# Kernel tuning notes

Hardware: AMD Instinct MI355X
Metric: run time of the kernel (lower is better)

## Reference

```python
import jax, jax.numpy as jnp
import numpy as np

B, V, E = 32, 2048, 12288
IMG_F = 512
GCN_DIMS = [(3 + IMG_F, 512), (512, 512), (512, 512), (512, 512), (512, 64), (64, 3)]
FC_DIMS = [(V * 3, 1024), (1024, 1024), (1024, V * 3)]


def setup_inputs() -> dict:
    key = jax.random.key(0)
    ks = jax.random.split(key, 3 + len(GCN_DIMS) + len(FC_DIMS))
    inp = {}
    inp["vertices"] = jax.random.normal(ks[0], (B, V, 3), dtype=jnp.float32)
    inp["img_features"] = jax.random.normal(ks[1], (B, IMG_F), dtype=jnp.float32)
    inp["edge_index"] = jax.random.randint(ks[2], (2, E), 0, V, dtype=jnp.int32)
    for i, (fi, fo) in enumerate(GCN_DIMS):
        inp[f"W{i+1}"] = (jax.random.normal(ks[3 + i], (fi, fo), dtype=jnp.float32) / np.sqrt(fi)).astype(jnp.float32)
        inp[f"b{i+1}"] = jnp.zeros((fo,), dtype=jnp.float32)
    for i, (fi, fo) in enumerate(FC_DIMS):
        inp[f"fcW{i+1}"] = (jax.random.normal(ks[3 + len(GCN_DIMS) + i], (fi, fo), dtype=jnp.float32) / np.sqrt(fi)).astype(jnp.float32)
        inp[f"fcb{i+1}"] = jnp.zeros((fo,), dtype=jnp.float32)
    return inp


def _gcn_norm(edge_index):
    # PyG GCNConv: add self-loops, symmetric normalization 1/sqrt(d_i d_j).
    loop = jnp.arange(V, dtype=edge_index.dtype)
    src = jnp.concatenate([edge_index[0], loop])
    dst = jnp.concatenate([edge_index[1], loop])
    deg = jax.ops.segment_sum(jnp.ones_like(dst, dtype=jnp.float32), dst, num_segments=V)
    dinv = jax.lax.rsqrt(deg)  # deg >= 1 due to self-loops
    norm = dinv[src] * dinv[dst]  # [E+V]
    return src, dst, norm


def _gcn_layer(x, W, b, src, dst, norm):
    # x: [B, V, Fin] -> [B, V, Fout]; transform then gather/scatter aggregate.
    h = jnp.einsum("bvi,io->bvo", x, W)
    msg = h[:, src, :] * norm[None, :, None]          # gather over edges
    agg = jax.vmap(lambda m: jax.ops.segment_sum(m, dst, num_segments=V))(msg)
    return agg + b


def reference(vertices, img_features, edge_index,
              W1, b1, W2, b2, W3, b3, W4, b4, W5, b5, W6, b6,
              fcW1, fcb1, fcW2, fcb2, fcW3, fcb3):
    src, dst, norm = _gcn_norm(edge_index)
    # concat vertex coords with broadcast image feature: [B, V, 3+512]
    x = jnp.concatenate([vertices, jnp.broadcast_to(img_features[:, None, :], (B, V, IMG_F))], axis=2)
    x = _gcn_layer(x, W1, b1, src, dst, norm)
    x = _gcn_layer(x, W2, b2, src, dst, norm)
    x = jax.nn.relu(x)
    x = _gcn_layer(x, W3, b3, src, dst, norm)
    x = _gcn_layer(x, W4, b4, src, dst, norm)
    x = jax.nn.relu(x)
    x = _gcn_layer(x, W5, b5, src, dst, norm)
    x = _gcn_layer(x, W6, b6, src, dst, norm)
    x = jax.nn.relu(x)
    x = x.reshape(B, V * 3)
    h = x @ fcW1 + fcb1
    h = h @ fcW2 + fcb2
    h = jnp.tanh(h @ fcW3 + fcb3)
    deformations = h.reshape(B, V, 3) * 0.1
    return vertices + deformations
```

## Files before the change

### kernel.cpp

```cpp
#include <hip/hip_runtime.h>
#include <stdint.h>
#include <math.h>

#define B_ 32
#define V_ 2048
#define E_ 12288
#define M_ (B_*V_)

typedef __bf16 bf16x8 __attribute__((ext_vector_type(8)));
typedef float f32x4 __attribute__((ext_vector_type(4)));

__device__ __forceinline__ float bf2f(unsigned short u){
  union { unsigned int i; float f; } v; v.i = ((unsigned int)u) << 16; return v.f;
}
__device__ __forceinline__ unsigned short f2bf(float f){
  union { float f; unsigned int i; } v; v.f = f;
  unsigned int r = (v.i + 0x7fffu + ((v.i >> 16) & 1u)) >> 16;
  return (unsigned short)r;
}
__device__ __forceinline__ void gload16(const unsigned short* g, unsigned short* l){
  __builtin_amdgcn_global_load_lds(
      (const __attribute__((address_space(1))) void*)g,
      (__attribute__((address_space(3))) void*)l, 16, 0, 0);
}

__global__ __launch_bounds__(1024) void k_pre0(
    const int* __restrict__ ei, int* __restrict__ rowptr_g, int* __restrict__ cols_g,
    float* __restrict__ vals_g, float* __restrict__ selfw_g,
    float* __restrict__ wsum_g, float* __restrict__ w2_g,
    const float* __restrict__ W3, const float* __restrict__ W4,
    const float* __restrict__ img, const float* __restrict__ W1,
    unsigned short* __restrict__ W3B, unsigned short* __restrict__ W4T,
    float* __restrict__ partB){
  __shared__ int   sdeg[V_];
  __shared__ int   srp[V_ + 1];
  __shared__ int   sfill[V_];
  __shared__ float sdinv[V_];
  __shared__ float swsum[V_];
  __shared__ float sw2[V_];
  __shared__ int   swt[16];
  __shared__ __align__(16) float tile[4][32][33];
  if (blockIdx.x == 0){
    const int t = threadIdx.x;
    sdeg[2*t] = 0; sdeg[2*t+1] = 0; sfill[2*t] = 0; sfill[2*t+1] = 0;
    __syncthreads();
    #pragma unroll
    for (int e = t; e < E_; e += 1024) atomicAdd(&sdeg[ei[E_ + e]], 1);
    __syncthreads();
    int c0 = sdeg[2*t], c1 = sdeg[2*t+1];
    int s2 = c0 + c1;
    int lane = t & 63, wid = t >> 6;
    int pre = s2;
    #pragma unroll
    for (int off = 1; off < 64; off <<= 1){
      int u = __shfl_up(pre, off);
      if (lane >= off) pre += u;
    }
    if (lane == 63) swt[wid] = pre;
    __syncthreads();
    if (t == 0){
      int run = 0;
      #pragma unroll
      for (int i = 0; i < 16; i++){ int x = swt[i]; swt[i] = run; run += x; }
      srp[V_] = run;
    }
    __syncthreads();
    int base = swt[wid] + (pre - s2);
    srp[2*t] = base; srp[2*t+1] = base + c0;
    #pragma unroll
    for (int v = t; v < V_; v += 1024){
      float d = (float)(sdeg[v] + 1);
      float di = rsqrtf(d);
      sdinv[v] = di;
      swsum[v] = di * di;
    }
    __syncthreads();
    #pragma unroll
    for (int e = t; e < E_; e += 1024){
      int s = ei[e], d = ei[E_ + e];
      int pos = srp[d] + atomicAdd(&sfill[d], 1);
      float val = sdinv[s] * sdinv[d];
      cols_g[pos] = s;
      vals_g[pos] = val;
      atomicAdd(&swsum[d], val);
    }
    __syncthreads();
    #pragma unroll
    for (int v = t; v < V_; v += 1024)
      sw2[v] = (sdinv[v] * sdinv[v]) * swsum[v];
    __syncthreads();
    #pragma unroll
    for (int e = t; e < E_; e += 1024){
      int s = ei[e], d = ei[E_ + e];
      atomicAdd(&sw2[d], sdinv[s] * sdinv[d] * swsum[s]);
    }
    __syncthreads();
    #pragma unroll
    for (int v = t; v < V_; v += 1024){
      rowptr_g[v] = srp[v];
      selfw_g[v]  = sdinv[v] * sdinv[v];
      wsum_g[v]   = swsum[v];
      w2_g[v]     = sw2[v];
    }
    if (t == 0) rowptr_g[V_] = srp[V_];
  } else {
    int u = blockIdx.x - 1;
    int t10 = threadIdx.x;
    int sub = (u << 2) + (t10 >> 8);
    int t = t10 & 255;
    int ti = t10 >> 8;
    if (sub < 256){
      int tr0 = (sub >> 4) << 5, tc0 = (sub & 15) << 5;
      int r = t >> 5, c = t & 31;
      #pragma unroll
      for (int i = 0; i < 4; i++)
        tile[ti][r + 8*i][c] = W4[(size_t)(tr0 + r + 8*i) * 512 + tc0 + c];
      __syncthreads();
      #pragma unroll
      for (int i = 0; i < 4; i++)
        W4T[(size_t)(tc0 + r + 8*i) * 512 + tr0 + c] = f2bf(tile[ti][c][r + 8*i]);
    } else if (sub < 256 + 1024){
      int id = (sub - 256) * 256 + t;
      W3B[id] = f2bf(W3[id]);
    } else {
      int g = sub - 1280;
      int kc = g >> 1, nh = g & 1;
      int k0 = kc * 16;
      float* xs = &tile[ti][0][0];
      for (int i = t; i < 512; i += 256)
        xs[i] = img[(size_t)(i >> 4) * 512 + k0 + (i & 15)];
      __syncthreads();
      const float* W = W1 + 3 * 512;
      int n = (nh << 8) + t;
      float acc[32] = {};
      #pragma unroll
      for (int kg = 0; kg < 4; kg++){
        const float* wp = W + (size_t)(k0 + kg * 4) * 512 + n;
        float w0 = wp[0], w1 = wp[512], w2 = wp[1024], w3 = wp[1536];
        #pragma unroll
        for (int r = 0; r < 32; r++){
          f32x4 xv = *(const f32x4*)&xs[r * 16 + kg * 4];
          acc[r] += xv[0]*w0 + xv[1]*w1 + xv[2]*w2 + xv[3]*w3;
        }
      }
      float* p = partB + (size_t)kc * 16384 + n;
      #pragma unroll
      for (int r = 0; r < 32; r++) p[(size_t)r * 512] = acc[r];
    }
  }
}

__global__ __launch_bounds__(256) void k_preB(
    const float* __restrict__ partB, float* __restrict__ I1,
    const float* __restrict__ b3, const float* __restrict__ W4,
    const float* __restrict__ W5, const float* __restrict__ W6,
    const float* __restrict__ b5,
    float* __restrict__ C34, float* __restrict__ W56, float* __restrict__ C56){
  int blk = blockIdx.x, t = threadIdx.x;
  if (blk < 64){
    int id = blk * 256 + t;
    float a = 0.f;
    #pragma unroll
    for (int s = 0; s < 32; s++) a += partB[(size_t)s * 16384 + id];
    I1[id] = a;
  } else {
    int id = (blk - 64) * 256 + t;
    if (id < 512){
      float a0=0,a1=0,a2=0,a3=0;
      for (int k = 0; k < 512; k += 4){
        a0 += b3[k]   * W4[(size_t)k * 512 + id];
        a1 += b3[k+1] * W4[(size_t)(k+1) * 512 + id];
        a2 += b3[k+2] * W4[(size_t)(k+2) * 512 + id];
        a3 += b3[k+3] * W4[(size_t)(k+3) * 512 + id];
      }
      C34[id] = a0+a1+a2+a3;
    } else if (id < 512 + 1536){
      int i = id - 512; int k5 = i / 3, j = i % 3;
      float a = 0.f;
      #pragma unroll 4
      for (int u = 0; u < 64; u++) a += W5[k5 * 64 + u] * W6[u * 3 + j];
      W56[i] = a;
    } else if (id < 512 + 1536 + 3){
      int j = id - (512 + 1536);
      float a = 0.f;
      #pragma unroll 4
      for (int u = 0; u < 64; u++) a += b5[u] * W6[u * 3 + j];
      C56[j] = a;
    }
  }
}

__global__ __launch_bounds__(256) void k_preC(
    const float* __restrict__ b1, const float* __restrict__ W1,
    const float* __restrict__ I1, const float* __restrict__ W2,
    float* __restrict__ partB){
  __shared__ __align__(16) float xs[36 * 16];
  int g = blockIdx.x;
  int kc = g >> 1, k0 = kc * 16;
  int t = threadIdx.x;
  int n = ((g & 1) << 8) + t;
  for (int i = t; i < 576; i += 256){
    int r = i >> 4, kk = i & 15;
    const float* q;
    if (r == 0)      q = b1;
    else if (r < 4)  q = W1 + (size_t)(r - 1) * 512;
    else             q = I1 + (size_t)(r - 4) * 512;
    xs[i] = q[k0 + kk];
  }
  __syncthreads();
  float acc[36] = {};
  #pragma unroll
  for (int kg = 0; kg < 4; kg++){
    const float* wp = W2 + (size_t)(k0 + kg * 4) * 512 + n;
    float w0 = wp[0], w1 = wp[512], w2 = wp[1024], w3 = wp[1536];
    #pragma unroll
    for (int r = 0; r < 36; r++){
      f32x4 xv = *(const f32x4*)&xs[r * 16 + kg * 4];
      acc[r] += xv[0]*w0 + xv[1]*w1 + xv[2]*w2 + xv[3]*w3;
    }
  }
  float* p = partB + (size_t)kc * 18432 + n;
  #pragma unroll
  for (int r = 0; r < 36; r++) p[(size_t)r * 512] = acc[r];
}

__global__ __launch_bounds__(256) void k_preD(
    const float* __restrict__ partB, float* __restrict__ P){
  int id = blockIdx.x * 256 + threadIdx.x;
  float a = 0.f;
  #pragma unroll
  for (int s = 0; s < 32; s++) a += partB[(size_t)s * 18432 + id];
  P[id] = a;
}

__global__ __launch_bounds__(1024) void k_va2(
    const float* __restrict__ in, const int* __restrict__ rowptr,
    const int* __restrict__ cols, const float* __restrict__ vals,
    const float* __restrict__ selfw, float* __restrict__ outv){
  __shared__ float xs[V_ * 3];
  __shared__ float ys[V_ * 3];
  int b = blockIdx.x, t = threadIdx.x;
  const float* ib = in + (size_t)b * V_ * 3;
  for (int i = t; i < V_ * 3; i += 1024) xs[i] = ib[i];
  __syncthreads();
  for (int v = t; v < V_; v += 1024){
    float sw = selfw[v];
    float a0 = sw * xs[v*3], a1 = sw * xs[v*3+1], a2 = sw * xs[v*3+2];
    int re = rowptr[v + 1];
    for (int e = rowptr[v]; e < re; e++){
      int s = cols[e]; float vv = vals[e];
      a0 += vv * xs[s*3]; a1 += vv * xs[s*3+1]; a2 += vv * xs[s*3+2];
    }
    ys[v*3] = a0; ys[v*3+1] = a1; ys[v*3+2] = a2;
  }
  __syncthreads();
  for (int v = t; v < V_; v += 1024){
    float sw = selfw[v];
    float a0 = sw * ys[v*3], a1 = sw * ys[v*3+1], a2 = sw * ys[v*3+2];
    int re = rowptr[v + 1];
    for (int e = rowptr[v]; e < re; e++){
      int s = cols[e]; float vv = vals[e];
      a0 += vv * ys[s*3]; a1 += vv * ys[s*3+1]; a2 += vv * ys[s*3+2];
    }
    float* o = outv + ((size_t)v * 32 + b) * 3;
    o[0] = a0; o[1] = a1; o[2] = a2;
  }
}

__global__ __launch_bounds__(1024) void k_x2(
    const float* __restrict__ va2v, const float* __restrict__ P,
    const float* __restrict__ wsum, const float* __restrict__ w2s,
    const float* __restrict__ b2,
    unsigned short* __restrict__ Y){
  int v = (blockIdx.x << 2) + (threadIdx.x >> 8);
  int batch = (blockIdx.y << 2) + ((threadIdx.x >> 6) & 3);
  int f8 = (threadIdx.x & 63) * 8;
  const float* va = va2v + ((size_t)v * 32 + batch) * 3;
  float x0 = va[0], x1 = va[1], x2 = va[2];
  float w2v = w2s[v], wsv = wsum[v];
  float tt[8];
  #pragma unroll
  for (int h = 0; h < 2; h++){
    f32x4 wv0 = *(const f32x4*)&P[512  + f8 + 4*h];
    f32x4 wv1 = *(const f32x4*)&P[1024 + f8 + 4*h];
    f32x4 wv2 = *(const f32x4*)&P[1536 + f8 + 4*h];
    f32x4 ccv = *(const f32x4*)&P[f8 + 4*h];
    f32x4 bbv = *(const f32x4*)&b2[f8 + 4*h];
    f32x4 iiv = *(const f32x4*)&P[2048 + (size_t)batch * 512 + f8 + 4*h];
    #pragma unroll
    for (int j = 0; j < 4; j++){
      float tv = x0*wv0[j] + x1*wv1[j] + x2*wv2[j] + w2v*iiv[j] + wsv*ccv[j] + bbv[j];
      tt[4*h + j] = fmaxf(tv, 0.f);
    }
  }
  unsigned int o[4];
  #pragma unroll
  for (int i = 0; i < 4; i++)
    o[i] = (unsigned int)f2bf(tt[2*i]) | ((unsigned int)f2bf(tt[2*i+1]) << 16);
  *(uint4*)&Y[((size_t)v * 32 + batch) * 512 + f8] = *(uint4*)o;
}

__global__ __launch_bounds__(256) void k_aggb(
    const unsigned short* __restrict__ Hg, const int* __restrict__ rowptr,
    const int* __restrict__ cols, const float* __restrict__ vals,
    const float* __restrict__ selfw, unsigned short* __restrict__ Xo){
  int dst = blockIdx.x;
  int batch = (blockIdx.y << 2) + (threadIdx.x >> 6);
  int f8 = (threadIdx.x & 63) * 8;
  int rs = rowptr[dst], re = rowptr[dst + 1];
  float sw = selfw[dst];
  float a[8];
  {
    uint4 q = *(const uint4*)&Hg[((size_t)dst * 32 + batch) * 512 + f8];
    const unsigned int* w = (const unsigned int*)&q;
    #pragma unroll
    for (int i = 0; i < 4; i++){
      a[2*i]   = sw * bf2f(w[i] & 0xffff);
      a[2*i+1] = sw * bf2f(w[i] >> 16);
    }
  }
  int e = rs;
  for (; e + 1 < re; e += 2){
    int s0 = cols[e], s1 = cols[e+1];
    float v0 = vals[e], v1 = vals[e+1];
    uint4 q0 = *(const uint4*)&Hg[((size_t)s0 * 32 + batch) * 512 + f8];
    uint4 q1 = *(const uint4*)&Hg[((size_t)s1 * 32 + batch) * 512 + f8];
    const unsigned int* w0 = (const unsigned int*)&q0;
    const unsigned int* w1 = (const unsigned int*)&q1;
    #pragma unroll
    for (int i = 0; i < 4; i++){
      a[2*i]   += v0 * bf2f(w0[i] & 0xffff) + v1 * bf2f(w1[i] & 0xffff);
      a[2*i+1] += v0 * bf2f(w0[i] >> 16)    + v1 * bf2f(w1[i] >> 16);
    }
  }
  if (e < re){
    int s = cols[e]; float v = vals[e];
    uint4 q = *(const uint4*)&Hg[((size_t)s * 32 + batch) * 512 + f8];
    const unsigned int* w = (const unsigned int*)&q;
    #pragma unroll
    for (int i = 0; i < 4; i++){
      a[2*i]   += v * bf2f(w[i] & 0xffff);
      a[2*i+1] += v * bf2f(w[i] >> 16);
    }
  }
  unsigned int o[4];
  #pragma unroll
  for (int i = 0; i < 4; i++)
    o[i] = (unsigned int)f2bf(a[2*i]) | ((unsigned int)f2bf(a[2*i+1]) << 16);
  *(uint4*)&Xo[((size_t)dst * 32 + batch) * 512 + f8] = *(uint4*)o;
}

template<int BM, int BN, int WM, int WN, int TM, int TN>
__global__ __launch_bounds__(WM*WN*64) void k_gemm(
    const unsigned short* __restrict__ Xg, const unsigned short* __restrict__ Wt,
    unsigned short* __restrict__ Hg, int K, int N,
    const float* __restrict__ wsumv, const float* __restrict__ cvec,
    const float* __restrict__ bias, int relu,
    const float* __restrict__ W56g, float* __restrict__ h5p){
  constexpr int BK = 32;
  constexpr int NW = WM * WN;
  constexpr int NT = NW * 64;
  constexpr int RA = BM / NW;
  constexpr int RB = BN / NW;
  __shared__ __align__(16) unsigned short As[2][BM * BK];
  __shared__ __align__(16) unsigned short Bs[2][BN * BK];
  __shared__ float h5s[BM * 3];
  const int tid = threadIdx.x;
  const int row0 = blockIdx.x * BM, col0 = blockIdx.y * BN;
  const int wave = tid >> 6, lane = tid & 63;
  const int wr = wave / WN, wc = wave % WN;
  const int lrow = lane & 15, lq = lane >> 4;
  const int lrw = lane >> 2, lcol = (lane & 3) * 8;
  const int arow = wave * RA, brow = wave * RB;
  if (h5p){
    for (int i = tid; i < BM * 3; i += NT) h5s[i] = 0.f;
  }
  f32x4 acc[TM][TN] = {};
  #pragma unroll
  for (int t = 0; t < RA / 16; t++)
    gload16(&Xg[(size_t)(row0 + arow + t * 16 + lrw) * K + lcol],
            &As[0][(arow + t * 16) * BK]);
  #pragma unroll
  for (int t = 0; t < RB / 16; t++)
    gload16(&Wt[(size_t)(col0 + brow + t * 16 + lrw) * K + lcol],
            &Bs[0][(brow + t * 16) * BK]);
  int cur = 0;
  for (int k0 = 0; k0 < K; k0 += BK){
    __syncthreads();
    if (k0 + BK < K){
      #pragma unroll
      for (int t = 0; t < RA / 16; t++)
        gload16(&Xg[(size_t)(row0 + arow + t * 16 + lrw) * K + k0 + BK + lcol],
                &As[cur ^ 1][(arow + t * 16) * BK]);
      #pragma unroll
      for (int t = 0; t < RB / 16; t++)
        gload16(&Wt[(size_t)(col0 + brow + t * 16 + lrw) * K + k0 + BK + lcol],
                &Bs[cur ^ 1][(brow + t * 16) * BK]);
    }
    bf16x8 af[TM], bfr[TN];
    #pragma unroll
    for (int tm = 0; tm < TM; tm++)
      af[tm] = *(const bf16x8*)&As[cur][(wr * TM * 16 + tm * 16 + lrow) * BK + lq * 8];
    #pragma unroll
    for (int tn = 0; tn < TN; tn++)
      bfr[tn] = *(const bf16x8*)&Bs[cur][(wc * TN * 16 + tn * 16 + lrow) * BK + lq * 8];
    #pragma unroll
    for (int tm = 0; tm < TM; tm++)
      #pragma unroll
      for (int tn = 0; tn < TN; tn++)
        acc[tm][tn] = __builtin_amdgcn_mfma_f32_16x16x32_bf16(af[tm], bfr[tn], acc[tm][tn], 0, 0, 0);
    cur ^= 1;
  }
  if (h5p){
    float w56l[TN][3], cvl[TN], bvl[TN];
    #pragma unroll
    for (int tn = 0; tn < TN; tn++){
      int col = col0 + wc * TN * 16 + tn * 16 + lrow;
      cvl[tn] = cvec[col]; bvl[tn] = bias[col];
      w56l[tn][0] = W56g[col * 3];
      w56l[tn][1] = W56g[col * 3 + 1];
      w56l[tn][2] = W56g[col * 3 + 2];
    }
    #pragma unroll
    for (int tm = 0; tm < TM; tm++){
      #pragma unroll
      for (int r = 0; r < 4; r++){
        int lr = wr * TM * 16 + tm * 16 + lq * 4 + r;
        float ws = wsumv[(row0 + lr) >> 5];
        float p0 = 0.f, p1 = 0.f, p2 = 0.f;
        #pragma unroll
        for (int tn = 0; tn < TN; tn++){
          float x = fmaxf(acc[tm][tn][r] + ws * cvl[tn] + bvl[tn], 0.f);
          p0 += x * w56l[tn][0]; p1 += x * w56l[tn][1]; p2 += x * w56l[tn][2];
        }
        #pragma unroll
        for (int off = 8; off; off >>= 1){
          p0 += __shfl_down(p0, off);
          p1 += __shfl_down(p1, off);
          p2 += __shfl_down(p2, off);
        }
        if (lrow == 0){
          atomicAdd(&h5s[lr * 3 + 0], p0);
          atomicAdd(&h5s[lr * 3 + 1], p1);
          atomicAdd(&h5s[lr * 3 + 2], p2);
        }
      }
    }
    __syncthreads();
    float* dst = h5p + (size_t)blockIdx.y * ((size_t)M_ * 3) + (size_t)row0 * 3;
    for (int i = tid; i < BM * 3; i += NT) dst[i] = h5s[i];
  } else {
    #pragma unroll
    for (int tm = 0; tm < TM; tm++){
      #pragma unroll
      for (int tn = 0; tn < TN; tn++){
        int col = col0 + wc * TN * 16 + tn * 16 + lrow;
        float cv = 0.f, bv = 0.f;
        if (cvec){ cv = cvec[col]; bv = bias[col]; }
        #pragma unroll
        for (int r = 0; r < 4; r++){
          int row = row0 + wr * TM * 16 + tm * 16 + lq * 4 + r;
          float x = acc[tm][tn][r];
          if (cvec) x += wsumv[row >> 5] * cv + bv;
          if (relu) x = fmaxf(x, 0.f);
          Hg[(size_t)row * N + col] = f2bf(x);
        }
      }
    }
  }
}

__global__ __launch_bounds__(1024) void k_xa2(
    const float* __restrict__ h5p, const int* __restrict__ rowptr,
    const int* __restrict__ cols, const float* __restrict__ vals,
    const float* __restrict__ selfw, const float* __restrict__ wsum,
    const float* __restrict__ C56, const float* __restrict__ b6,
    float* __restrict__ XF){
  __shared__ float xs[V_ * 3];
  __shared__ float ys[V_ * 3];
  int b = blockIdx.x, t = threadIdx.x;
  const size_t M3 = (size_t)M_ * 3;
  for (int i = t; i < V_ * 3; i += 1024){
    int v = i / 3, j = i - v * 3;
    size_t g = ((size_t)v * 32 + b) * 3 + j;
    xs[i] = h5p[g] + h5p[M3 + g] + h5p[2 * M3 + g] + h5p[3 * M3 + g];
  }
  __syncthreads();
  for (int v = t; v < V_; v += 1024){
    float sw = selfw[v];
    float a0 = sw * xs[v*3], a1 = sw * xs[v*3+1], a2 = sw * xs[v*3+2];
    int re = rowptr[v + 1];
    for (int e = rowptr[v]; e < re; e++){
      int s = cols[e]; float vv = vals[e];
      a0 += vv * xs[s*3]; a1 += vv * xs[s*3+1]; a2 += vv * xs[s*3+2];
    }
    ys[v*3] = a0; ys[v*3+1] = a1; ys[v*3+2] = a2;
  }
  __syncthreads();
  float* ob = XF + (size_t)b * V_ * 3;
  for (int v = t; v < V_; v += 1024){
    float sw = selfw[v];
    float a0 = sw * ys[v*3], a1 = sw * ys[v*3+1], a2 = sw * ys[v*3+2];
    int re = rowptr[v + 1];
    for (int e = rowptr[v]; e < re; e++){
      int s = cols[e]; float vv = vals[e];
      a0 += vv * ys[s*3]; a1 += vv * ys[s*3+1]; a2 += vv * ys[s*3+2];
    }
    float w = wsum[v];
    a0 = fmaxf(a0 + w * C56[0] + b6[0], 0.f);
    a1 = fmaxf(a1 + w * C56[1] + b6[1], 0.f);
    a2 = fmaxf(a2 + w * C56[2] + b6[2], 0.f);
    ob[v*3] = a0; ob[v*3+1] = a1; ob[v*3+2] = a2;
  }
}

template<int R, int KC>
__global__ __launch_bounds__(256) void k_fcp(
    const float* __restrict__ in, const float* __restrict__ W,
    float* __restrict__ partial, int K, int N){
  const int n = blockIdx.x * 256 + threadIdx.x;
  const int k0 = blockIdx.y * KC;
  float acc[R] = {};
  for (int kk = 0; kk < KC; kk += 4){
    const float* wp = W + (size_t)(k0 + kk) * N + n;
    float w0 = wp[0];
    float w1 = wp[(size_t)N];
    float w2 = wp[(size_t)2 * N];
    float w3 = wp[(size_t)3 * N];
    #pragma unroll
    for (int r = 0; r < R; r++){
      const float* xp = in + (size_t)r * K + k0 + kk;
      acc[r] += xp[0]*w0 + xp[1]*w1 + xp[2]*w2 + xp[3]*w3;
    }
  }
  float* p = partial + (size_t)blockIdx.y * R * N + n;
  #pragma unroll
  for (int r = 0; r < R; r++) p[(size_t)r * N] = acc[r];
}

__global__ __launch_bounds__(256) void k_fcr(
    const float* __restrict__ partial, const float* __restrict__ bias,
    float* __restrict__ out, int total, int N, int KS, int mode,
    const float* __restrict__ vert){
  int id = blockIdx.x * 256 + threadIdx.x;
  if (id >= total) return;
  int n = id % N;
  float a0 = 0.f, a1 = 0.f, a2 = 0.f, a3 = 0.f;
  int s = 0;
  for (; s + 4 <= KS; s += 4){
    a0 += partial[(size_t)s * total + id];
    a1 += partial[(size_t)(s + 1) * total + id];
    a2 += partial[(size_t)(s + 2) * total + id];
    a3 += partial[(size_t)(s + 3) * total + id];
  }
  for (; s < KS; s++) a0 += partial[(size_t)s * total + id];
  float acc = a0 + a1 + a2 + a3;
  if (bias) acc += bias[n];
  if (mode) acc = vert[id] + 0.1f * tanhf(acc);
  out[id] = acc;
}

static constexpr size_t AL(size_t x){ return (x + 255) & ~(size_t)255; }
static constexpr size_t S512 = (size_t)M_ * 512 * 2;
static constexpr size_t S3   = (size_t)M_ * 3 * 4;
static constexpr size_t OXA  = 0;
static constexpr size_t OXB  = OXA  + AL(S512);
static constexpr size_t OVA2 = OXB  + AL(S512);
static constexpr size_t OH5P = OVA2 + AL(S3);
static constexpr size_t OXF  = OH5P + AL(4 * S3);
static constexpr size_t OFC1 = OXF  + AL(S3);
static constexpr size_t OFC2 = OFC1 + AL((size_t)B_ * 1024 * 4);
static constexpr size_t OI1  = OFC2 + AL((size_t)B_ * 1024 * 4);
static constexpr size_t OP   = OI1  + AL((size_t)32 * 512 * 4);
static constexpr size_t OC34 = OP   + AL((size_t)36 * 512 * 4);
static constexpr size_t OW56 = OC34 + AL((size_t)512 * 4);
static constexpr size_t OC56 = OW56 + AL((size_t)512 * 3 * 4);
static constexpr size_t OW3B = OC56 + AL((size_t)3 * 4);
static constexpr size_t OW4T = OW3B + AL((size_t)512 * 512 * 2);
static constexpr size_t OW34 = OW4T + AL((size_t)512 * 512 * 2);
static constexpr size_t OROW = OW34 + AL((size_t)512 * 512 * 2);
static constexpr size_t OCOL = OROW + AL((size_t)(V_ + 1) * 4);
static constexpr size_t OVAL = OCOL + AL((size_t)E_ * 4);
static constexpr size_t OSELF= OVAL + AL((size_t)E_ * 4);
static constexpr size_t OWS  = OSELF+ AL((size_t)V_ * 4);
static constexpr size_t OW2S = OWS  + AL((size_t)V_ * 4);

extern "C" void kernel_launch(void* const* d_in, const int* in_sizes, int n_in,
                              void* d_out, int out_size, void* d_ws, size_t ws_size,
                              hipStream_t stream){
  const float* vert  = (const float*)d_in[0];
  const float* img   = (const float*)d_in[1];
  const int*   ei    = (const int*)  d_in[2];
  const float* W1 = (const float*)d_in[3],  *b1 = (const float*)d_in[4];
  const float* W2 = (const float*)d_in[5],  *b2 = (const float*)d_in[6];
  const float* W3 = (const float*)d_in[7],  *b3 = (const float*)d_in[8];
  const float* W4 = (const float*)d_in[9],  *b4 = (const float*)d_in[10];
  const float* W5 = (const float*)d_in[11], *b5 = (const float*)d_in[12];
  const float* W6 = (const float*)d_in[13], *b6 = (const float*)d_in[14];
  const float* fcW1 = (const float*)d_in[15], *fcb1 = (const float*)d_in[16];
  const float* fcW2 = (const float*)d_in[17], *fcb2 = (const float*)d_in[18];
  const float* fcW3 = (const float*)d_in[19], *fcb3 = (const float*)d_in[20];
  float* out = (float*)d_out;

  char* ws = (char*)d_ws;
  unsigned short* XA  = (unsigned short*)(ws + OXA);
  unsigned short* XB  = (unsigned short*)(ws + OXB);
  float* VA2v = (float*)(ws + OVA2);
  float* H5P  = (float*)(ws + OH5P);
  float* XF   = (float*)(ws + OXF);
  float* FC1o = (float*)(ws + OFC1);
  float* FC2o = (float*)(ws + OFC2);
  float* I1   = (float*)(ws + OI1);
  float* P    = (float*)(ws + OP);
  float* C34  = (float*)(ws + OC34);
  float* W56  = (float*)(ws + OW56);
  float* C56  = (float*)(ws + OC56);
  unsigned short* W3B = (unsigned short*)(ws + OW3B);
  unsigned short* W4T = (unsigned short*)(ws + OW4T);
  unsigned short* W34 = (unsigned short*)(ws + OW34);
  float* PARTA = (float*)(ws + OXA);
  float* PARTB = (float*)(ws + OXB);
  int*   ROW  = (int*)(ws + OROW);
  int*   COL  = (int*)(ws + OCOL);
  float* VAL  = (float*)(ws + OVAL);
  float* SELF = (float*)(ws + OSELF);
  float* WSUM = (float*)(ws + OWS);
  float* W2S  = (float*)(ws + OW2S);

  k_pre0<<<337, 1024, 0, stream>>>(ei, ROW, COL, VAL, SELF, WSUM, W2S,
                                   W3, W4, img, W1, W3B, W4T, PARTB);
  k_preB<<<64 + 9, 256, 0, stream>>>(PARTB, I1, b3, W4, W5, W6, b5, C34, W56, C56);
  k_preC<<<64, 256, 0, stream>>>(b1, W1, I1, W2, PARTB);
  k_preD<<<72, 256, 0, stream>>>(PARTB, P);
  k_gemm<64,64,2,2,2,2><<<dim3(8, 8), 256, 0, stream>>>(W4T, W3B, W34, 512, 512,
                                                        nullptr, nullptr, nullptr, 0,
                                                        nullptr, nullptr);

  k_va2<<<B_, 1024, 0, stream>>>(vert, ROW, COL, VAL, SELF, VA2v);
  k_x2<<<dim3(V_ / 4, 8), 1024, 0, stream>>>(VA2v, P, WSUM, W2S, b2, XA);
  k_aggb<<<dim3(V_, 8), 256, 0, stream>>>(XA, ROW, COL, VAL, SELF, XB);
  k_aggb<<<dim3(V_, 8), 256, 0, stream>>>(XB, ROW, COL, VAL, SELF, XA);

  k_gemm<128,128,2,2,4,4><<<dim3(M_ / 128, 4), 256, 0, stream>>>(XA, W34, XB, 512, 512,
                                                                 WSUM, C34, b4, 1,
                                                                 W56, H5P);

  k_xa2<<<B_, 1024, 0, stream>>>(H5P, ROW, COL, VAL, SELF, WSUM, C56, b6, XF);

  k_fcp<32,64><<<dim3(4, 96), 256, 0, stream>>>(XF, fcW1, PARTA, 6144, 1024);
  k_fcr<<<(B_ * 1024 + 255) / 256, 256, 0, stream>>>(PARTA, fcb1, FC1o, 32 * 1024, 1024, 96, 0, nullptr);
  k_fcp<32,64><<<dim3(4, 16), 256, 0, stream>>>(FC1o, fcW2, PARTA, 1024, 1024);
  k_fcr<<<(B_ * 1024 + 255) / 256, 256, 0, stream>>>(PARTA, fcb2, FC2o, 32 * 1024, 1024, 16, 0, nullptr);
  k_fcp<32,64><<<dim3(24, 16), 256, 0, stream>>>(FC2o, fcW3, PARTA, 1024, 6144);
  k_fcr<<<(B_ * 6144 + 255) / 256, 256, 0, stream>>>(PARTA, fcb3, out, 32 * 6144, 6144, 16, 1, vert);
}
```

Baseline: 582.7 us.

## Fuse two sparse aggregation passes into one LDS-resident kernel per feature chunk

Replaces the two back-to-back global-memory gather/scatter aggregation launches with a single kernel. Each block loads a 16-feature slice for one batch across all vertices into LDS, runs both aggregation hops out of shared memory, and writes only the final result. This removes the intermediate global round trip and the random global gathers. In exchange it uses 128KB of LDS per 1024-thread block, which limits occupancy, and each block walks the full CSR once per hop.

```diff
diff --git a/kernel.cpp b/kernel.cpp
--- a/kernel.cpp
+++ b/kernel.cpp
@@ -300,54 +300,110 @@
   *(uint4*)&Y[((size_t)v * 32 + batch) * 512 + f8] = *(uint4*)o;
 }
 
-__global__ __launch_bounds__(256) void k_aggb(
+__global__ __launch_bounds__(1024) void k_agg2(
     const unsigned short* __restrict__ Hg, const int* __restrict__ rowptr,
     const int* __restrict__ cols, const float* __restrict__ vals,
     const float* __restrict__ selfw, unsigned short* __restrict__ Xo){
-  int dst = blockIdx.x;
-  int batch = (blockIdx.y << 2) + (threadIdx.x >> 6);
-  int f8 = (threadIdx.x & 63) * 8;
-  int rs = rowptr[dst], re = rowptr[dst + 1];
-  float sw = selfw[dst];
-  float a[8];
-  {
-    uint4 q = *(const uint4*)&Hg[((size_t)dst * 32 + batch) * 512 + f8];
-    const unsigned int* w = (const unsigned int*)&q;
-    #pragma unroll
-    for (int i = 0; i < 4; i++){
-      a[2*i]   = sw * bf2f(w[i] & 0xffff);
-      a[2*i+1] = sw * bf2f(w[i] >> 16);
-    }
-  }
-  int e = rs;
-  for (; e + 1 < re; e += 2){
-    int s0 = cols[e], s1 = cols[e+1];
-    float v0 = vals[e], v1 = vals[e+1];
-    uint4 q0 = *(const uint4*)&Hg[((size_t)s0 * 32 + batch) * 512 + f8];
-    uint4 q1 = *(const uint4*)&Hg[((size_t)s1 * 32 + batch) * 512 + f8];
-    const unsigned int* w0 = (const unsigned int*)&q0;
-    const unsigned int* w1 = (const unsigned int*)&q1;
-    #pragma unroll
-    for (int i = 0; i < 4; i++){
-      a[2*i]   += v0 * bf2f(w0[i] & 0xffff) + v1 * bf2f(w1[i] & 0xffff);
-      a[2*i+1] += v0 * bf2f(w0[i] >> 16)    + v1 * bf2f(w1[i] >> 16);
-    }
-  }
-  if (e < re){
-    int s = cols[e]; float v = vals[e];
-    uint4 q = *(const uint4*)&Hg[((size_t)s * 32 + batch) * 512 + f8];
-    const unsigned int* w = (const unsigned int*)&q;
-    #pragma unroll
-    for (int i = 0; i < 4; i++){
-      a[2*i]   += v * bf2f(w[i] & 0xffff);
-      a[2*i+1] += v * bf2f(w[i] >> 16);
-    }
-  }
-  unsigned int o[4];
-  #pragma unroll
-  for (int i = 0; i < 4; i++)
-    o[i] = (unsigned int)f2bf(a[2*i]) | ((unsigned int)f2bf(a[2*i+1]) << 16);
-  *(uint4*)&Xo[((size_t)dst * 32 + batch) * 512 + f8] = *(uint4*)o;
+  __shared__ __align__(16) unsigned short xs[V_ * 16];
+  __shared__ __align__(16) unsigned short ys[V_ * 16];
+  const int fc = blockIdx.x;
+  const int b  = blockIdx.y;
+  const int t = threadIdx.x;
+  for (int i = t; i < V_ * 2; i += 1024){
+    int v = i >> 1, h = (i & 1) << 3;
+    *(uint4*)&xs[v * 16 + h] =
+        *(const uint4*)&Hg[((size_t)v * 32 + b) * 512 + fc * 16 + h];
+  }
+  __syncthreads();
+  for (int i = t; i < V_ * 2; i += 1024){
+    int dst = i >> 1, h = (i & 1) << 3;
+    float sw = selfw[dst];
+    float a[8];
+    {
+      uint4 q = *(const uint4*)&xs[dst * 16 + h];
+      const unsigned int* w = (const unsigned int*)&q;
+      #pragma unroll
+      for (int k = 0; k < 4; k++){
+        a[2*k]   = sw * bf2f(w[k] & 0xffff);
+        a[2*k+1] = sw * bf2f(w[k] >> 16);
+      }
+    }
+    int rs = rowptr[dst], re = rowptr[dst + 1];
+    int e = rs;
+    for (; e + 1 < re; e += 2){
+      int s0 = cols[e], s1 = cols[e+1];
+      float v0 = vals[e], v1 = vals[e+1];
+      uint4 q0 = *(const uint4*)&xs[s0 * 16 + h];
+      uint4 q1 = *(const uint4*)&xs[s1 * 16 + h];
+      const unsigned int* w0 = (const unsigned int*)&q0;
+      const unsigned int* w1 = (const unsigned int*)&q1;
+      #pragma unroll
+      for (int k = 0; k < 4; k++){
+        a[2*k]   += v0 * bf2f(w0[k] & 0xffff) + v1 * bf2f(w1[k] & 0xffff);
+        a[2*k+1] += v0 * bf2f(w0[k] >> 16)    + v1 * bf2f(w1[k] >> 16);
+      }
+    }
+    if (e < re){
+      int s = cols[e]; float v = vals[e];
+      uint4 q = *(const uint4*)&xs[s * 16 + h];
+      const unsigned int* w = (const unsigned int*)&q;
+      #pragma unroll
+      for (int k = 0; k < 4; k++){
+        a[2*k]   += v * bf2f(w[k] & 0xffff);
+        a[2*k+1] += v * bf2f(w[k] >> 16);
+      }
+    }
+    unsigned int o[4];
+    #pragma unroll
+    for (int k = 0; k < 4; k++)
+      o[k] = (unsigned int)f2bf(a[2*k]) | ((unsigned int)f2bf(a[2*k+1]) << 16);
+    *(uint4*)&ys[dst * 16 + h] = *(uint4*)o;
+  }
+  __syncthreads();
+  for (int i = t; i < V_ * 2; i += 1024){
+    int dst = i >> 1, h = (i & 1) << 3;
+    float sw = selfw[dst];
+    float a[8];
+    {
+      uint4 q = *(const uint4*)&ys[dst * 16 + h];
+      const unsigned int* w = (const unsigned int*)&q;
+      #pragma unroll
+      for (int k = 0; k < 4; k++){
+        a[2*k]   = sw * bf2f(w[k] & 0xffff);
+        a[2*k+1] = sw * bf2f(w[k] >> 16);
+      }
+    }
+    int rs = rowptr[dst], re = rowptr[dst + 1];
+    int e = rs;
+    for (; e + 1 < re; e += 2){
+      int s0 = cols[e], s1 = cols[e+1];
+      float v0 = vals[e], v1 = vals[e+1];
+      uint4 q0 = *(const uint4*)&ys[s0 * 16 + h];
+      uint4 q1 = *(const uint4*)&ys[s1 * 16 + h];
+      const unsigned int* w0 = (const unsigned int*)&q0;
+      const unsigned int* w1 = (const unsigned int*)&q1;
+      #pragma unroll
+      for (int k = 0; k < 4; k++){
+        a[2*k]   += v0 * bf2f(w0[k] & 0xffff) + v1 * bf2f(w1[k] & 0xffff);
+        a[2*k+1] += v0 * bf2f(w0[k] >> 16)    + v1 * bf2f(w1[k] >> 16);
+      }
+    }
+    if (e < re){
+      int s = cols[e]; float v = vals[e];
+      uint4 q = *(const uint4*)&ys[s * 16 + h];
+      const unsigned int* w = (const unsigned int*)&q;
+      #pragma unroll
+      for (int k = 0; k < 4; k++){
+        a[2*k]   += v * bf2f(w[k] & 0xffff);
+        a[2*k+1] += v * bf2f(w[k] >> 16);
+      }
+    }
+    unsigned int o[4];
+    #pragma unroll
+    for (int k = 0; k < 4; k++)
+      o[k] = (unsigned int)f2bf(a[2*k]) | ((unsigned int)f2bf(a[2*k+1]) << 16);
+    *(uint4*)&Xo[((size_t)dst * 32 + b) * 512 + fc * 16 + h] = *(uint4*)o;
+  }
 }
 
 template<int BM, int BN, int WM, int WN, int TM, int TN>
@@ -638,10 +694,9 @@
 
   k_va2<<<B_, 1024, 0, stream>>>(vert, ROW, COL, VAL, SELF, VA2v);
   k_x2<<<dim3(V_ / 4, 8), 1024, 0, stream>>>(VA2v, P, WSUM, W2S, b2, XA);
-  k_aggb<<<dim3(V_, 8), 256, 0, stream>>>(XA, ROW, COL, VAL, SELF, XB);
-  k_aggb<<<dim3(V_, 8), 256, 0, stream>>>(XB, ROW, COL, VAL, SELF, XA);
-
-  k_gemm<128,128,2,2,4,4><<<dim3(M_ / 128, 4), 256, 0, stream>>>(XA, W34, XB, 512, 512,
+  k_agg2<<<dim3(32, 32), 1024, 0, stream>>>(XA, ROW, COL, VAL, SELF, XB);
+
+  k_gemm<128,128,2,2,4,4><<<dim3(M_ / 128, 4), 256, 0, stream>>>(XB, W34, XA, 512, 512,
                                                                  WSUM, C34, b4, 1,
                                                                  W56, H5P);
 
```

Result: slower. 610.2 us (+4.7%).
